# Kernel tuning notes

Measured on AMD Instinct MI355X. Metric: run time of the kernel, lower is better.

## Reference

```python
import jax, jax.numpy as jnp
import numpy as np

# ---- DNC configuration (mirrors access_config / controller_config / args) ----
T, B, IN, OUT = 64, 32, 64, 64          # time, batch, input_size, output_size
N, Wd, R, NW = 128, 64, 4, 1            # memory_size, word_size, num_reads, num_writes
H = 256                                  # controller hidden_size (2 LSTM layers)
CLIP = 20.0
EPS = 1e-6
NUM_MODES = 2 * NW + 1                   # backward modes, forward modes, content mode
IF_SIZES = [R*Wd, R, NW*Wd, NW, NW*Wd, NW*Wd, R, NW, NW, R*NUM_MODES]
IF_SIZE = int(np.sum(IF_SIZES))


def setup_inputs() -> dict:
    key = jax.random.key(0)
    ks = jax.random.split(key, 12)
    in0 = IN + R * Wd  # controller input = external input + flattened prev reads

    def w(k, shape, fan):
        return jax.random.normal(k, shape, jnp.float32) / np.float32(np.sqrt(fan))

    return {
        "inputs": jax.random.normal(ks[0], (T, B, IN), jnp.float32),
        "Wx0": w(ks[1], (in0, 4 * H), in0),
        "Wh0": w(ks[2], (H, 4 * H), H),
        "b0": jnp.zeros((4 * H,), jnp.float32),
        "Wx1": w(ks[3], (H, 4 * H), H),
        "Wh1": w(ks[4], (H, 4 * H), H),
        "b1": jnp.zeros((4 * H,), jnp.float32),
        "W_if": w(ks[5], (H, IF_SIZE), H),
        "b_if": jnp.zeros((IF_SIZE,), jnp.float32),
        "W_out": w(ks[6], (H + R * Wd, OUT), H + R * Wd),
        "b_out": jnp.zeros((OUT,), jnp.float32),
    }


def _lstm(x, h, c, Wx, Wh, b):
    g = x @ Wx + h @ Wh + b
    i, f, gg, o = jnp.split(g, 4, axis=-1)
    c2 = jax.nn.sigmoid(f) * c + jax.nn.sigmoid(i) * jnp.tanh(gg)
    h2 = jax.nn.sigmoid(o) * jnp.tanh(c2)
    return h2, c2


def _content_weights(memory, keys, strengths):
    # memory [B,N,W], keys [B,h,W], strengths [B,h] -> [B,h,N]
    mnorm = jnp.linalg.norm(memory, axis=-1)          # [B,N]
    knorm = jnp.linalg.norm(keys, axis=-1)            # [B,h]
    dot = jnp.einsum('bhw,bnw->bhn', keys, memory)
    sim = dot / (knorm[..., None] * mnorm[:, None, :] + EPS)
    return jax.nn.softmax(sim * strengths[..., None], axis=-1)


def _allocation(usage):
    # usage [B,N] -> allocation weighting [B,N] (DNC freeness-based)
    usage = EPS + (1.0 - EPS) * usage
    order = jnp.argsort(usage, axis=-1)               # ascending usage (most free first)
    sorted_usage = jnp.take_along_axis(usage, order, axis=-1)
    prod = jnp.cumprod(sorted_usage, axis=-1)
    prod_excl = jnp.concatenate([jnp.ones_like(prod[:, :1]), prod[:, :-1]], axis=-1)
    alloc_sorted = (1.0 - sorted_usage) * prod_excl
    inv = jnp.argsort(order, axis=-1)
    return jnp.take_along_axis(alloc_sorted, inv, axis=-1)


def _dnc_forward(inputs, Wx0, Wh0, b0, Wx1, Wh1, b1, W_if, b_if, W_out, b_out):
    eye = 1.0 - jnp.eye(N, dtype=jnp.float32)
    splits = np.cumsum(IF_SIZES)[:-1]

    def step(state, x_t):
        h0, c0, h1, c1, M, rw, ww, link, prec, usage, reads = state
        ctrl_in = jnp.concatenate([x_t, reads.reshape(B, R * Wd)], axis=-1)
        h0, c0 = _lstm(ctrl_in, h0, c0, Wx0, Wh0, b0)
        h1, c1 = _lstm(h0, h1, c1, Wx1, Wh1, b1)
        ctrl = jnp.clip(h1, -CLIP, CLIP)

        p = jnp.split(ctrl @ W_if + b_if, splits, axis=-1)
        read_keys = p[0].reshape(B, R, Wd)
        read_str = 1.0 + jax.nn.softplus(p[1])              # oneplus
        write_keys = p[2].reshape(B, NW, Wd)
        write_str = 1.0 + jax.nn.softplus(p[3])
        erase = jax.nn.sigmoid(p[4]).reshape(B, NW, Wd)
        write_vec = p[5].reshape(B, NW, Wd)
        free_g = jax.nn.sigmoid(p[6])                       # [B,R]
        alloc_g = jax.nn.sigmoid(p[7])                      # [B,NW]
        write_g = jax.nn.sigmoid(p[8])                      # [B,NW]
        modes = jax.nn.softmax(p[9].reshape(B, R, NUM_MODES), axis=-1)

        # -- usage update (prev write weights, then free gates on prev reads) --
        cw = 1.0 - jnp.prod(1.0 - ww, axis=1)               # [B,N]
        u = usage + (1.0 - usage) * cw
        psi = jnp.prod(1.0 - free_g[..., None] * rw, axis=1)
        usage = u * psi

        # -- write weights: content + allocation, gated --
        wc = _content_weights(M, write_keys, write_str)     # [B,NW,N]
        u_tmp = usage
        ww_heads = []
        for i in range(NW):
            a = _allocation(u_tmp)
            wg = write_g[:, i:i+1]
            ag = alloc_g[:, i:i+1]
            ww_heads.append(wg * (ag * a + (1.0 - ag) * wc[:, i]))
            u_tmp = u_tmp + (1.0 - u_tmp) * wg * a
        ww = jnp.stack(ww_heads, axis=1)                    # [B,NW,N]

        # -- erase + write memory --
        erase_m = jnp.prod(1.0 - ww[..., None] * erase[:, :, None, :], axis=1)  # [B,N,W]
        add_m = jnp.einsum('bwn,bwk->bnk', ww, write_vec)
        M = M * erase_m + add_m

        # -- temporal link matrix + precedence --
        wi = ww[..., :, None]
        wj = ww[..., None, :]
        link = ((1.0 - wi - wj) * link + wi * prec[..., None, :]) * eye
        prec = (1.0 - ww.sum(axis=-1, keepdims=True)) * prec + ww

        # -- read weights: backward / content / forward modes --
        rc = _content_weights(M, read_keys, read_str)       # [B,R,N]
        fwd = jnp.einsum('bwij,brj->brwi', link, rw)
        bwd = jnp.einsum('bwji,brj->brwi', link, rw)
        bmode = modes[..., :NW]
        fmode = modes[..., NW:2*NW]
        cmode = modes[..., 2*NW]
        rw = (jnp.einsum('brw,brwn->brn', bmode, bwd)
              + cmode[..., None] * rc
              + jnp.einsum('brw,brwn->brn', fmode, fwd))
        reads = jnp.einsum('brn,bnk->brk', rw, M)           # [B,R,W]

        out = jnp.clip(jnp.concatenate([ctrl, reads.reshape(B, R * Wd)], axis=-1) @ W_out + b_out,
                       -CLIP, CLIP)
        return (h0, c0, h1, c1, M, rw, ww, link, prec, usage, reads), out

    z = jnp.zeros
    init = (z((B, H)), z((B, H)), z((B, H)), z((B, H)),
            z((B, N, Wd)), z((B, R, N)), z((B, NW, N)),
            z((B, NW, N, N)), z((B, NW, N)), z((B, N)), z((B, R, Wd)))
    _, outs = jax.lax.scan(step, init, inputs)
    return outs                                            # [T,B,OUT]


def reference(inputs, Wx0, Wh0, b0, Wx1, Wh1, b1, W_if, b_if, W_out, b_out):
    return _dnc_forward(inputs, Wx0, Wh0, b0, Wx1, Wh1, b1, W_if, b_if, W_out, b_out)
```

## Files before the change

kernel.cpp:

```cpp
#include <hip/hip_runtime.h>
#include <math.h>


#define TT   64
#define BB   32
#define INW  64
#define OUTW 64
#define NN   128
#define WD   64
#define RR   4
#define HH   256
#define IFSZ 471
#define CLIPV 20.0f
#define EPSV  1e-6f
#define NBLK 96

#define OFF_RK   0
#define OFF_RSTR 256
#define OFF_WK   260
#define OFF_WSTR 324
#define OFF_ER   325
#define OFF_WV   389
#define OFF_FG   453
#define OFF_AG   457
#define OFF_WG   458
#define OFF_MD   459

#define S_WSTR 0
#define S_AG   1
#define S_WG   2
#define S_KNW  3
#define S_WSUM 4
#define S_RSTR 8
#define S_FG   12
#define S_KNR  16
#define S_BM   20
#define S_FM   24
#define S_CM   28

#define A_XS   0
#define A_GL   11840
#define A_C0   12896
#define A_GO   13152
#define A_WS   13216
#define A_WO   34528
#define B_XS   0
#define B_GL   9472
#define B_C1   10528
#define B_W1   10784
#define C_MS   0
#define C_LS   8320
#define C_WW   24832
#define C_PRC  24960
#define C_USG  25088
#define C_RWS  25216
#define C_IFC  25728
#define C_FWD  26208
#define C_BWD  26720
#define C_U2   27232
#define C_WCS  27360
#define C_RCS  27488
#define C_MNO  28000
#define C_RDS  28128
#define C_ERS  28384
#define C_WVS  28448
#define C_SC   28512
#define C_SCAL 28576

#define SMEM_FLOATS 36064
#define SMEM_BYTES  (SMEM_FLOATS*4)

#define W_CTL  0
#define W_RDS  8192
#define W_H0   16384
#define W_H1   32768
#define W_FLA  49152
#define W_FLB  (W_FLA + 1024)
#define W_FLC  (W_FLB + 1024)
#define W_END  (W_FLC + 1024)

__device__ __forceinline__ float sigf(float x){ return 1.0f/(1.0f+expf(-x)); }
__device__ __forceinline__ float sofp(float x){ return fmaxf(x,0.0f)+log1pf(expf(-fabsf(x))); }

__device__ __forceinline__ float gload(const float* p){
  return __hip_atomic_load(p, __ATOMIC_RELAXED, __HIP_MEMORY_SCOPE_AGENT);
}
__device__ __forceinline__ void gstore(float* p, float v){
  __hip_atomic_store(p, v, __ATOMIC_RELAXED, __HIP_MEMORY_SCOPE_AGENT);
}

__device__ __forceinline__ void waitflag(const unsigned* slots, unsigned target){
  if (threadIdx.x < 64){
    for (;;){
      unsigned m = __hip_atomic_load(&slots[(threadIdx.x & 31)*32],
                                     __ATOMIC_RELAXED, __HIP_MEMORY_SCOPE_AGENT);
      #pragma unroll
      for (int s=32;s>0;s>>=1){
        unsigned o = (unsigned)__shfl_xor((int)m, s, 64);
        m = (o < m) ? o : m;
      }
      if (m >= target) break;
      __builtin_amdgcn_s_sleep(2);
    }
  }
  __syncthreads();
}

__device__ __forceinline__ void setflag(unsigned* slots, int g, unsigned val){
  asm volatile("s_waitcnt vmcnt(0)" ::: "memory");
  __syncthreads();
  if (threadIdx.x == 0)
    __hip_atomic_store(&slots[g*32], val, __ATOMIC_RELAXED, __HIP_MEMORY_SCOPE_AGENT);
}

__device__ __forceinline__ float wredSum(float v){
  #pragma unroll
  for (int m=32;m>0;m>>=1) v += __shfl_xor(v,m,64);
  return v;
}
__device__ __forceinline__ float wredMax(float v){
  #pragma unroll
  for (int m=32;m>0;m>>=1) v = fmaxf(v,__shfl_xor(v,m,64));
  return v;
}

__device__ __forceinline__ float bfly64(float (&A)[64], int l, int* jb){
  #pragma unroll
  for (int st=0; st<6; ++st){
    const int m = 1<<st, half = 32>>st;
    const bool hi = (l & m) != 0;
    #pragma unroll
    for (int j=0;j<half;j++){
      float a = A[j], b = A[j+half];
      float keep = hi? b : a;
      float send = hi? a : b;
      A[j] = keep + __shfl_xor(send, m, 64);
    }
  }
  *jb = ((l&1)?32:0)|((l&2)?16:0)|((l&4)?8:0)|((l&8)?4:0)|((l&16)?2:0)|((l&32)?1:0);
  return A[0];
}

#define TILE_FMA(WBASE, WROW, XROW)                                      \
  {                                                                      \
    float xv[8], wv[8];                                                  \
    _Pragma("unroll")                                                    \
    for (int q=0;q<8;q++){                                               \
      wv[q] = sm[(WBASE) + (WROW)*37 + c0 + q];                          \
      xv[q] = Xs[(XROW)*37 + b0 + q];                                    \
    }                                                                    \
    _Pragma("unroll")                                                    \
    for (int bi=0;bi<8;bi++)                                             \
      _Pragma("unroll")                                                  \
      for (int ci=0;ci<8;ci++)                                           \
        acc[bi*8+ci] += xv[bi]*wv[ci];                                   \
  }

extern "C" __global__ __launch_bounds__(1024, 1)
void dnc_coop8(const float* __restrict__ inputs,
               const float* __restrict__ Wx0, const float* __restrict__ Wh0, const float* __restrict__ b0g,
               const float* __restrict__ Wx1, const float* __restrict__ Wh1, const float* __restrict__ b1g,
               const float* __restrict__ Wifg, const float* __restrict__ bifg,
               const float* __restrict__ Woutg, const float* __restrict__ boutg,
               float* __restrict__ outg, float* __restrict__ ws)
{
  const int bid  = blockIdx.x;
  const int role = bid >> 5;
  const int g    = bid & 31;
  const int tid  = threadIdx.x;
  const int lane = tid & 63;
  const int wid  = tid >> 6;

  extern __shared__ float sm[];

  float* gctl  = ws + W_CTL;
  float* greads= ws + W_RDS;
  unsigned* fA = (unsigned*)(ws + W_FLA);
  unsigned* fB = (unsigned*)(ws + W_FLB);
  unsigned* fC = (unsigned*)(ws + W_FLC);

  if (role == 0){
    for (int i = tid; i < 576*32; i += 1024){
      int r = i >> 5, cl = i & 31;
      int cglob = 8*g + (cl&7) + ((cl>>3)<<8);
      float v;
      if (r < 256)      v = Wx0[(64+r)*1024 + cglob];
      else if (r < 320) v = Wx0[(r-256)*1024 + cglob];
      else              v = Wh0[(r-320)*1024 + cglob];
      sm[A_WS + r*37 + cl] = v;
    }
    for (int i = tid; i < 512*2; i += 1024){
      int k = i >> 1, c = i & 1;
      sm[A_WO + k*3 + c] = Woutg[k*64 + 2*g + c];
    }
    if (tid < 256) sm[A_C0 + tid] = 0.0f;
  } else if (role == 1){
    for (int i = tid; i < 512*32; i += 1024){
      int r = i >> 5, cl = i & 31;
      int cglob = 8*g + (cl&7) + ((cl>>3)<<8);
      sm[B_W1 + r*37 + cl] = (r < 256) ? Wx1[r*1024 + cglob]
                                       : Wh1[(r-256)*1024 + cglob];
    }
    if (tid < 256) sm[B_C1 + tid] = 0.0f;
  } else {
    for (int i = tid; i < NN*65;  i += 1024) sm[C_MS + i] = 0.0f;
    for (int i = tid; i < NN*129; i += 1024) sm[C_LS + i] = 0.0f;
    if (tid < 128){ sm[C_WW+tid]=0.f; sm[C_PRC+tid]=0.f; sm[C_USG+tid]=0.f; }
    if (tid < 512) sm[C_RWS+tid]=0.f;
  }
  __syncthreads();

  if (role == 0){
    float* Xs = sm + A_XS;
    for (int t = 0; t <= TT; ++t){
      float* h0old = ws + W_H0 + (t&1)*8192;
      float* h0new = ws + W_H0 + ((t+1)&1)*8192;
      float acc[64]; float accO[16];

      waitflag(fA, (unsigned)t);
      if (t < TT){
        for (int i = tid; i < 256*32; i += 1024){
          int k = i>>5, bb = i&31; Xs[k*37+bb] = gload(&h0old[i]);
        }
        for (int i = tid; i < 64*32; i += 1024){
          int bb = i>>6, k = i&63;
          Xs[(256+k)*37+bb] = inputs[(t*BB + bb)*INW + k];
        }
        __syncthreads();
        #pragma unroll
        for (int j=0;j<64;j++) acc[j]=0.f;
        {
          const int b0 = (wid>>2)*8, c0 = (wid&3)*8;
          #pragma unroll
          for (int i=0;i<4;i++){
            int k = i*64 + lane;
            TILE_FMA(A_WS, 320+k, k)
          }
          TILE_FMA(A_WS, 256+lane, 256+lane)
        }
        __syncthreads();
      }
      if (t > 0){
        waitflag(fB, (unsigned)t);
        for (int i = tid; i < 256*32; i += 1024){
          int k = i>>5, bb = i&31; Xs[k*37+bb] = gload(&gctl[i]);
        }
        __syncthreads();
        #pragma unroll
        for (int j=0;j<16;j++) accO[j]=0.f;
        if (wid < 4){
          const int b0 = wid*8;
          #pragma unroll
          for (int i=0;i<4;i++){
            int k = i*64 + lane;
            float w0 = sm[A_WO + k*3], w1 = sm[A_WO + k*3 + 1];
            float xv[8];
            #pragma unroll
            for (int q=0;q<8;q++) xv[q] = Xs[k*37 + b0 + q];
            #pragma unroll
            for (int bi=0;bi<8;bi++){
              accO[bi*2]   += xv[bi]*w0;
              accO[bi*2+1] += xv[bi]*w1;
            }
          }
        }
        __syncthreads();
      }
      waitflag(fC, (unsigned)t);
      for (int i = tid; i < 256*32; i += 1024){
        int k = i>>5, bb = i&31; Xs[k*37+bb] = gload(&greads[i]);
      }
      __syncthreads();
      if (t > 0){
        if (wid < 4){
          const int b0 = wid*8;
          #pragma unroll
          for (int i=0;i<4;i++){
            int k = i*64 + lane;
            float w0 = sm[A_WO + (256+k)*3], w1 = sm[A_WO + (256+k)*3 + 1];
            float xv[8];
            #pragma unroll
            for (int q=0;q<8;q++) xv[q] = Xs[k*37 + b0 + q];
            #pragma unroll
            for (int bi=0;bi<8;bi++){
              accO[bi*2]   += xv[bi]*w0;
              accO[bi*2+1] += xv[bi]*w1;
            }
          }
          #pragma unroll
          for (int st=0; st<4; ++st){
            const int m = 1<<st, half = 8>>st;
            const bool hi = (lane & m) != 0;
            #pragma unroll
            for (int j=0;j<half;j++){
              float a = accO[j], b = accO[j+half];
              float keep = hi? b : a;
              float send = hi? a : b;
              accO[j] = keep + __shfl_xor(send, m, 64);
            }
          }
          accO[0] += __shfl_xor(accO[0], 16, 64);
          accO[0] += __shfl_xor(accO[0], 32, 64);
          int jb = ((lane&1)?8:0)|((lane&2)?4:0)|((lane&4)?2:0)|((lane&8)?1:0);
          if ((lane & 48) == 0){
            int bi = jb>>1, ci = jb&1;
            sm[A_GO + (wid*8+bi)*2 + ci] = accO[0];
          }
        }
        __syncthreads();
        if (tid < 64){
          int bb = tid>>1, c = tid&1;
          float v = sm[A_GO + tid] + boutg[2*g + c];
          outg[((t-1)*BB + bb)*OUTW + 2*g + c] = fminf(CLIPV, fmaxf(-CLIPV, v));
        }
      }
      if (t == TT) break;
      {
        const int b0 = (wid>>2)*8, c0 = (wid&3)*8;
        #pragma unroll
        for (int i=0;i<4;i++){
          int k = i*64 + lane;
          TILE_FMA(A_WS, k, k)
        }
        int jb; float v = bfly64(acc, lane, &jb);
        sm[A_GL + (b0 + (jb>>3))*33 + c0 + (jb&7)] = v;
      }
      __syncthreads();
      if (tid < 256){
        int bb = tid>>3, j = tid&7;
        float gi = sm[A_GL + bb*33 + j]      + b0g[8*g + j];
        float gf = sm[A_GL + bb*33 + 8 + j]  + b0g[256 + 8*g + j];
        float gg = sm[A_GL + bb*33 + 16 + j] + b0g[512 + 8*g + j];
        float go = sm[A_GL + bb*33 + 24 + j] + b0g[768 + 8*g + j];
        float c = sigf(gf)*sm[A_C0+tid] + sigf(gi)*tanhf(gg);
        sm[A_C0+tid] = c;
        gstore(&h0new[(8*g + j)*32 + bb], sigf(go)*tanhf(c));
      }
      setflag(fA, g, (unsigned)(t+1));
    }
  } else if (role == 1){
    float* Xs = sm + B_XS;
    for (int t = 0; t < TT; ++t){
      float* h0new = ws + W_H0 + ((t+1)&1)*8192;
      float* h1old = ws + W_H1 + (t&1)*8192;
      float* h1new = ws + W_H1 + ((t+1)&1)*8192;
      float acc[64];
      #pragma unroll
      for (int j=0;j<64;j++) acc[j]=0.f;

      waitflag(fB, (unsigned)t);
      for (int i = tid; i < 256*32; i += 1024){
        int k = i>>5, bb = i&31; Xs[k*37+bb] = gload(&h1old[i]);
      }
      __syncthreads();
      {
        const int b0 = (wid>>2)*8, c0 = (wid&3)*8;
        #pragma unroll
        for (int i=0;i<4;i++){
          int k = i*64 + lane;
          TILE_FMA(B_W1, 256+k, k)
        }
      }
      __syncthreads();
      waitflag(fA, (unsigned)(t+1));
      for (int i = tid; i < 256*32; i += 1024){
        int k = i>>5, bb = i&31; Xs[k*37+bb] = gload(&h0new[i]);
      }
      __syncthreads();
      {
        const int b0 = (wid>>2)*8, c0 = (wid&3)*8;
        #pragma unroll
        for (int i=0;i<4;i++){
          int k = i*64 + lane;
          TILE_FMA(B_W1, k, k)
        }
        int jb; float v = bfly64(acc, lane, &jb);
        sm[B_GL + (b0 + (jb>>3))*33 + c0 + (jb&7)] = v;
      }
      __syncthreads();
      if (tid < 256){
        int bb = tid>>3, j = tid&7;
        float gi = sm[B_GL + bb*33 + j]      + b1g[8*g + j];
        float gf = sm[B_GL + bb*33 + 8 + j]  + b1g[256 + 8*g + j];
        float gg = sm[B_GL + bb*33 + 16 + j] + b1g[512 + 8*g + j];
        float go = sm[B_GL + bb*33 + 24 + j] + b1g[768 + 8*g + j];
        float c = sigf(gf)*sm[B_C1+tid] + sigf(gi)*tanhf(gg);
        sm[B_C1+tid] = c;
        float h = sigf(go)*tanhf(c);
        gstore(&h1new[(8*g + j)*32 + bb], h);
        gstore(&gctl[(8*g + j)*32 + bb], fminf(CLIPV, fmaxf(-CLIPV, h)));
      }
      setflag(fB, g, (unsigned)(t+1));
    }
  } else {
    float* Ms  = sm + C_MS;
    float* Ls  = sm + C_LS;
    float* wws = sm + C_WW;
    float* prc = sm + C_PRC;
    float* usg = sm + C_USG;
    float* rws = sm + C_RWS;
    float* ifcl= sm + C_IFC;
    float* fwds= sm + C_FWD;
    float* bwds= sm + C_BWD;
    float* u2  = sm + C_U2;
    float* wcs = sm + C_WCS;
    float* rcs = sm + C_RCS;
    float* mno = sm + C_MNO;
    float* rds = sm + C_RDS;
    float* ers = sm + C_ERS;
    float* wvs = sm + C_WVS;
    float* sc  = sm + C_SC;
    float* scal= sm + C_SCAL;
    float* ctl_l = sm + C_RCS;
    float* part  = sm + C_FWD;

    for (int t = 0; t < TT; ++t){
      if (tid < 128){
        int n=tid; float s=0.f;
        #pragma unroll 8
        for (int d=0;d<WD;d++){ float v=Ms[n*65+d]; s+=v*v; }
        mno[n]=sqrtf(s);
      }
      waitflag(fB, (unsigned)(t+1));
      if (tid < 256) ctl_l[tid] = gload(&gctl[tid*32 + g]);
      __syncthreads();
      {
        const int kq = tid >> 9, c = tid & 511;
        if (c < IFSZ){
          const float* Wp = Wifg + (size_t)(kq*128)*IFSZ + c;
          const float* xp = ctl_l + kq*128;
          float a0=0.f, a1=0.f;
          #pragma unroll 8
          for (int k=0;k<128;k+=2){
            a0 += xp[k]   * Wp[(size_t)k*IFSZ];
            a1 += xp[k+1] * Wp[(size_t)(k+1)*IFSZ];
          }
          part[kq*512 + c] = a0 + a1;
        }
      }
      __syncthreads();
      if (tid < IFSZ) ifcl[tid] = part[tid] + part[512+tid] + bifg[tid];
      __syncthreads();

      if (tid < RR){
        scal[S_RSTR+tid]=1.0f+sofp(ifcl[OFF_RSTR+tid]);
        scal[S_FG+tid]  =sigf(ifcl[OFF_FG+tid]);
        float m0=ifcl[OFF_MD+tid*3], m1=ifcl[OFF_MD+tid*3+1], m2=ifcl[OFF_MD+tid*3+2];
        float mx=fmaxf(m0,fmaxf(m1,m2));
        float e0=expf(m0-mx), e1=expf(m1-mx), e2=expf(m2-mx);
        float s=e0+e1+e2;
        scal[S_BM+tid]=e0/s; scal[S_FM+tid]=e1/s; scal[S_CM+tid]=e2/s;
      }
      if (tid == 4) scal[S_WSTR]=1.0f+sofp(ifcl[OFF_WSTR]);
      if (tid == 5) scal[S_AG]=sigf(ifcl[OFF_AG]);
      if (tid == 6) scal[S_WG]=sigf(ifcl[OFF_WG]);
      if (tid >= 64 && tid < 128){
        int d=tid-64;
        ers[d]=sigf(ifcl[OFF_ER+d]);
        wvs[d]=ifcl[OFF_WV+d];
      }
      if (wid == 8){
        float v=ifcl[OFF_WK+lane]; float s=wredSum(v*v);
        if (lane==0) scal[S_KNW]=sqrtf(s);
      }
      if (wid >= 10 && wid < 14){
        int r=wid-10; float v=ifcl[OFF_RK+r*WD+lane]; float s=wredSum(v*v);
        if (lane==0) scal[S_KNR+r]=sqrtf(s);
      }
      __syncthreads();
      if (tid < NN){
        float dot=0.f;
        #pragma unroll 8
        for (int d=0;d<WD;d++) dot += ifcl[OFF_WK+d]*Ms[tid*65+d];
        float sim = dot/(scal[S_KNW]*mno[tid]+EPSV);
        wcs[tid]=sim*scal[S_WSTR];
      }
      __syncthreads();
      if (tid < NN){ float mx=wredMax(wcs[tid]); if(lane==0) sc[wid]=mx; }
      __syncthreads();
      if (tid < NN){
        float mx=fmaxf(sc[0],sc[1]);
        float e=expf(wcs[tid]-mx);
        wcs[tid]=e;
        float s=wredSum(e); if(lane==0) sc[2+wid]=s;
      }
      __syncthreads();
      if (tid < NN) wcs[tid]=wcs[tid]/(sc[2]+sc[3]);
      __syncthreads();
      if (tid < NN){
        float cw = wws[tid];
        float u  = usg[tid] + (1.0f-usg[tid])*cw;
        float psi=1.0f;
        #pragma unroll
        for (int r=0;r<RR;r++) psi *= 1.0f - scal[S_FG+r]*rws[r*NN+tid];
        float us = u*psi;
        usg[tid]=us;
        u2[tid] = EPSV + (1.0f-EPSV)*us;
      }
      __syncthreads();
      if (tid < NN){
        float ui=u2[tid]; float p=1.0f;
        for (int j=0;j<NN;j++){
          float uj=u2[j];
          bool take = (uj<ui) || (uj==ui && j<tid);
          p *= take ? uj : 1.0f;
        }
        float a = (1.0f-ui)*p;
        float wwn = scal[S_WG]*( scal[S_AG]*a + (1.0f-scal[S_AG])*wcs[tid] );
        wws[tid]=wwn;
        float s=wredSum(wwn); if(lane==0) sc[wid]=s;
      }
      __syncthreads();
      if (tid==0) scal[S_WSUM]=sc[0]+sc[1];
      __syncthreads();
      #pragma unroll
      for (int i=0;i<8;i++){
        int el=tid+i*1024, n=el>>6, d=el&63;
        float w=wws[n];
        Ms[n*65+d] = Ms[n*65+d]*(1.0f - w*ers[d]) + w*wvs[d];
      }
      #pragma unroll
      for (int i=0;i<16;i++){
        int el=tid+i*1024, li=el>>7, lj=el&127;
        float v = (li==lj) ? 0.0f
                : (1.0f - wws[li] - wws[lj])*Ls[li*129+lj] + wws[li]*prc[lj];
        Ls[li*129+lj]=v;
      }
      __syncthreads();
      if (tid < NN) prc[tid] = (1.0f - scal[S_WSUM])*prc[tid] + wws[tid];
      if (tid >= 128 && tid < 256){
        int n=tid-128; float s=0.f;
        #pragma unroll 8
        for (int d=0;d<WD;d++){ float v=Ms[n*65+d]; s+=v*v; }
        mno[n]=sqrtf(s);
      }
      __syncthreads();
      if (tid < RR*NN){
        int r=tid>>7, n=tid&127;
        float dot=0.f;
        #pragma unroll 8
        for (int d=0;d<WD;d++) dot += ifcl[OFF_RK+r*WD+d]*Ms[n*65+d];
        float sim = dot/(scal[S_KNR+r]*mno[n]+EPSV);
        rcs[tid]=sim*scal[S_RSTR+r];
      }
      __syncthreads();
      if (tid < RR*NN){ float mx=wredMax(rcs[tid]); if(lane==0) sc[wid]=mx; }
      __syncthreads();
      if (tid < RR*NN){
        int r=tid>>7;
        float mx=fmaxf(sc[r*2],sc[r*2+1]);
        float e=expf(rcs[tid]-mx);
        rcs[tid]=e;
        float s=wredSum(e); if(lane==0) sc[8+wid]=s;
      }
      __syncthreads();
      if (tid < RR*NN){
        int r=tid>>7;
        rcs[tid]=rcs[tid]/(sc[8+r*2]+sc[9+r*2]);
      }
      __syncthreads();
      if (tid < RR*NN){
        int r=tid>>7, i=tid&127;
        float f=0.f, bw=0.f;
        const float* rwr = rws + r*NN;
        #pragma unroll 4
        for (int j=0;j<NN;j++){
          float rv=rwr[j];
          f  += Ls[i*129+j]*rv;
          bw += Ls[j*129+i]*rv;
        }
        fwds[tid]=f; bwds[tid]=bw;
      }
      __syncthreads();
      if (tid < RR*NN){
        int r=tid>>7;
        rws[tid] = scal[S_BM+r]*bwds[tid] + scal[S_CM+r]*rcs[tid] + scal[S_FM+r]*fwds[tid];
      }
      __syncthreads();
      if (tid < RR*WD){
        int r=tid>>6, d=tid&63;
        float s=0.f;
        #pragma unroll 8
        for (int n=0;n<NN;n++) s += rws[r*NN+n]*Ms[n*65+d];
        rds[tid]=s;
      }
      __syncthreads();
      if (tid < 256) gstore(&greads[tid*32 + g], rds[tid]);
      setflag(fC, g, (unsigned)(t+1));
    }
  }
}

extern "C" void kernel_launch(void* const* d_in, const int* in_sizes, int n_in,
                              void* d_out, int out_size, void* d_ws, size_t ws_size,
                              hipStream_t stream)
{
  const float* inputs=(const float*)d_in[0];
  const float* Wx0   =(const float*)d_in[1];
  const float* Wh0   =(const float*)d_in[2];
  const float* b0    =(const float*)d_in[3];
  const float* Wx1   =(const float*)d_in[4];
  const float* Wh1   =(const float*)d_in[5];
  const float* b1    =(const float*)d_in[6];
  const float* Wif   =(const float*)d_in[7];
  const float* bif   =(const float*)d_in[8];
  const float* Wout  =(const float*)d_in[9];
  const float* bout  =(const float*)d_in[10];
  float* out = (float*)d_out;
  float* ws  = (float*)d_ws;

  hipMemsetAsync(ws, 0, W_END * sizeof(float), stream);

  hipFuncSetAttribute((const void*)dnc_coop8,
                      hipFuncAttributeMaxDynamicSharedMemorySize, SMEM_BYTES);

  void* args[] = { (void*)&inputs, (void*)&Wx0, (void*)&Wh0, (void*)&b0,
                   (void*)&Wx1, (void*)&Wh1, (void*)&b1, (void*)&Wif,
                   (void*)&bif, (void*)&Wout, (void*)&bout, (void*)&out,
                   (void*)&ws };
  hipLaunchCooperativeKernel((void*)dnc_coop8, dim3(NBLK), dim3(1024),
                             args, SMEM_BYTES, stream);
}
```

Baseline: 3.352 ms.

## Move layer-0 LSTM update ahead of output projection and coalesce hidden-state stores

The layer-0 LSTM gate computation and flag signal for step t+1 now run before the output projection of step t, so the layer-1 blocks can start sooner. The output projection leaves the critical path of the pipeline. LSTM cell and hidden-state indexing is remapped so each block writes its 256 hidden values contiguously, giving coalesced global stores. The memory block now writes read vectors straight to global, dropping a shared-memory staging step and a barrier. The gate math reads shared memory with a different index pattern, which may change bank conflicts.

```diff
diff --git a/kernel.cpp b/kernel.cpp
--- a/kernel.cpp
+++ b/kernel.cpp
@@ -157,12 +157,12 @@
   }
 
 extern "C" __global__ __launch_bounds__(1024, 1)
-void dnc_coop8(const float* __restrict__ inputs,
-               const float* __restrict__ Wx0, const float* __restrict__ Wh0, const float* __restrict__ b0g,
-               const float* __restrict__ Wx1, const float* __restrict__ Wh1, const float* __restrict__ b1g,
-               const float* __restrict__ Wifg, const float* __restrict__ bifg,
-               const float* __restrict__ Woutg, const float* __restrict__ boutg,
-               float* __restrict__ outg, float* __restrict__ ws)
+void dnc_coop11(const float* __restrict__ inputs,
+                const float* __restrict__ Wx0, const float* __restrict__ Wh0, const float* __restrict__ b0g,
+                const float* __restrict__ Wx1, const float* __restrict__ Wh1, const float* __restrict__ b1g,
+                const float* __restrict__ Wifg, const float* __restrict__ bifg,
+                const float* __restrict__ Woutg, const float* __restrict__ boutg,
+                float* __restrict__ outg, float* __restrict__ ws)
 {
   const int bid  = blockIdx.x;
   const int role = bid >> 5;
@@ -271,6 +271,30 @@
         int k = i>>5, bb = i&31; Xs[k*37+bb] = gload(&greads[i]);
       }
       __syncthreads();
+      if (t < TT){
+        {
+          const int b0 = (wid>>2)*8, c0 = (wid&3)*8;
+          #pragma unroll
+          for (int i=0;i<4;i++){
+            int k = i*64 + lane;
+            TILE_FMA(A_WS, k, k)
+          }
+          int jb; float v = bfly64(acc, lane, &jb);
+          sm[A_GL + (b0 + (jb>>3))*33 + c0 + (jb&7)] = v;
+        }
+        __syncthreads();
+        if (tid < 256){
+          int j = tid>>5, bb = tid&31;
+          float gi = sm[A_GL + bb*33 + j]      + b0g[8*g + j];
+          float gf = sm[A_GL + bb*33 + 8 + j]  + b0g[256 + 8*g + j];
+          float gg = sm[A_GL + bb*33 + 16 + j] + b0g[512 + 8*g + j];
+          float go = sm[A_GL + bb*33 + 24 + j] + b0g[768 + 8*g + j];
+          float c = sigf(gf)*sm[A_C0 + j*32 + bb] + sigf(gi)*tanhf(gg);
+          sm[A_C0 + j*32 + bb] = c;
+          gstore(&h0new[256*g + tid], sigf(go)*tanhf(c));
+        }
+        setflag(fA, g, (unsigned)(t+1));
+      }
       if (t > 0){
         if (wid < 4){
           const int b0 = wid*8;
@@ -314,29 +338,6 @@
           outg[((t-1)*BB + bb)*OUTW + 2*g + c] = fminf(CLIPV, fmaxf(-CLIPV, v));
         }
       }
-      if (t == TT) break;
-      {
-        const int b0 = (wid>>2)*8, c0 = (wid&3)*8;
-        #pragma unroll
-        for (int i=0;i<4;i++){
-          int k = i*64 + lane;
-          TILE_FMA(A_WS, k, k)
-        }
-        int jb; float v = bfly64(acc, lane, &jb);
-        sm[A_GL + (b0 + (jb>>3))*33 + c0 + (jb&7)] = v;
-      }
-      __syncthreads();
-      if (tid < 256){
-        int bb = tid>>3, j = tid&7;
-        float gi = sm[A_GL + bb*33 + j]      + b0g[8*g + j];
-        float gf = sm[A_GL + bb*33 + 8 + j]  + b0g[256 + 8*g + j];
-        float gg = sm[A_GL + bb*33 + 16 + j] + b0g[512 + 8*g + j];
-        float go = sm[A_GL + bb*33 + 24 + j] + b0g[768 + 8*g + j];
-        float c = sigf(gf)*sm[A_C0+tid] + sigf(gi)*tanhf(gg);
-        sm[A_C0+tid] = c;
-        gstore(&h0new[(8*g + j)*32 + bb], sigf(go)*tanhf(c));
-      }
-      setflag(fA, g, (unsigned)(t+1));
     }
   } else if (role == 1){
     float* Xs = sm + B_XS;
@@ -379,16 +380,16 @@
       }
       __syncthreads();
       if (tid < 256){
-        int bb = tid>>3, j = tid&7;
+        int j = tid>>5, bb = tid&31;
         float gi = sm[B_GL + bb*33 + j]      + b1g[8*g + j];
         float gf = sm[B_GL + bb*33 + 8 + j]  + b1g[256 + 8*g + j];
         float gg = sm[B_GL + bb*33 + 16 + j] + b1g[512 + 8*g + j];
         float go = sm[B_GL + bb*33 + 24 + j] + b1g[768 + 8*g + j];
-        float c = sigf(gf)*sm[B_C1+tid] + sigf(gi)*tanhf(gg);
-        sm[B_C1+tid] = c;
+        float c = sigf(gf)*sm[B_C1 + j*32 + bb] + sigf(gi)*tanhf(gg);
+        sm[B_C1 + j*32 + bb] = c;
         float h = sigf(go)*tanhf(c);
-        gstore(&h1new[(8*g + j)*32 + bb], h);
-        gstore(&gctl[(8*g + j)*32 + bb], fminf(CLIPV, fmaxf(-CLIPV, h)));
+        gstore(&h1new[256*g + tid], h);
+        gstore(&gctl[256*g + tid], fminf(CLIPV, fmaxf(-CLIPV, h)));
       }
       setflag(fB, g, (unsigned)(t+1));
     }
@@ -406,7 +407,6 @@
     float* wcs = sm + C_WCS;
     float* rcs = sm + C_RCS;
     float* mno = sm + C_MNO;
-    float* rds = sm + C_RDS;
     float* ers = sm + C_ERS;
     float* wvs = sm + C_WVS;
     float* sc  = sm + C_SC;
@@ -416,10 +416,10 @@
 
     for (int t = 0; t < TT; ++t){
       if (tid < 128){
-        int n=tid; float s=0.f;
+        float s=0.f;
         #pragma unroll 8
-        for (int d=0;d<WD;d++){ float v=Ms[n*65+d]; s+=v*v; }
-        mno[n]=sqrtf(s);
+        for (int d=0;d<WD;d++){ float v=Ms[tid*65+d]; s+=v*v; }
+        mno[tid]=sqrtf(s);
       }
       waitflag(fB, (unsigned)(t+1));
       if (tid < 256) ctl_l[tid] = gload(&gctl[tid*32 + g]);
@@ -582,10 +582,8 @@
         float s=0.f;
         #pragma unroll 8
         for (int n=0;n<NN;n++) s += rws[r*NN+n]*Ms[n*65+d];
-        rds[tid]=s;
-      }
-      __syncthreads();
-      if (tid < 256) gstore(&greads[tid*32 + g], rds[tid]);
+        gstore(&greads[tid*32 + g], s);
+      }
       setflag(fC, g, (unsigned)(t+1));
     }
   }
@@ -611,13 +609,13 @@
 
   hipMemsetAsync(ws, 0, W_END * sizeof(float), stream);
 
-  hipFuncSetAttribute((const void*)dnc_coop8,
+  hipFuncSetAttribute((const void*)dnc_coop11,
                       hipFuncAttributeMaxDynamicSharedMemorySize, SMEM_BYTES);
 
   void* args[] = { (void*)&inputs, (void*)&Wx0, (void*)&Wh0, (void*)&b0,
                    (void*)&Wx1, (void*)&Wh1, (void*)&b1, (void*)&Wif,
                    (void*)&bif, (void*)&Wout, (void*)&bout, (void*)&out,
                    (void*)&ws };
-  hipLaunchCooperativeKernel((void*)dnc_coop8, dim3(NBLK), dim3(1024),
+  hipLaunchCooperativeKernel((void*)dnc_coop11, dim3(NBLK), dim3(1024),
                              args, SMEM_BYTES, stream);
 }
```

After: 3.135 ms. -6.5%, faster.
